# Optimization experiments

Measured on AMD Instinct MI355X. Metric: run time of the kernel, lower is better.

## Reference

```python
import jax, jax.numpy as jnp
import numpy as np

B, S, D, H, F = 16, 1024, 256, 8, 1024
HD = D // H  # head_dim = 32
EPS = 1e-5


def setup_inputs() -> dict:
    key = jax.random.key(0)
    ks = jax.random.split(key, 12)
    sc = 0.02
    return {
        "x":      jax.random.normal(ks[0], (B, S, D), dtype=jnp.float32),
        "gamma1": jnp.ones((S, D), dtype=jnp.float32),
        "beta1":  jnp.zeros((S, D), dtype=jnp.float32),
        "Wqkv":   jax.random.normal(ks[1], (3 * D, D), dtype=jnp.float32) * sc,
        "bqkv":   jnp.zeros((3 * D,), dtype=jnp.float32),
        "Wo":     jax.random.normal(ks[2], (D, D), dtype=jnp.float32) * sc,
        "bo":     jnp.zeros((D,), dtype=jnp.float32),
        "gamma2": jnp.ones((S, D), dtype=jnp.float32),
        "beta2":  jnp.zeros((S, D), dtype=jnp.float32),
        "W1":     jax.random.normal(ks[3], (F, D), dtype=jnp.float32) * sc,
        "b1":     jnp.zeros((F,), dtype=jnp.float32),
        "W2":     jax.random.normal(ks[4], (D, F), dtype=jnp.float32) * sc,
        "b2":     jnp.zeros((D,), dtype=jnp.float32),
    }


def _layernorm_2d(x, gamma, beta):
    # normalizes jointly over the last TWO dims (seq, d_model), biased variance
    mean = jnp.mean(x, axis=(-2, -1), keepdims=True)
    var = jnp.mean((x - mean) ** 2, axis=(-2, -1), keepdims=True)
    y = (x - mean) / jnp.sqrt(var + EPS)
    return gamma * y + beta


def _mha(x, Wqkv, bqkv, Wo, bo):
    b, s, d = x.shape
    qkv = x @ Wqkv.T + bqkv                                  # [B,S,3D]
    qkv = qkv.reshape(b, s, H, 3 * HD).transpose(0, 2, 1, 3)  # [B,H,S,3HD]
    q, k, v = jnp.split(qkv, 3, axis=-1)                      # each [B,H,S,HD]
    scores = jnp.einsum("bhqd,bhkd->bhqk", q, k) / np.sqrt(HD).astype(np.float32)
    attn = jax.nn.softmax(scores, axis=-1)                    # [B,H,S,S]
    values = jnp.einsum("bhqk,bhkd->bhqd", attn, v)           # [B,H,S,HD]
    # NOTE: original torch code reshapes (B,H,S,HD)->(B,S,H*HD) WITHOUT permuting
    # back; we faithfully reproduce that (row-major reshape, same as torch).
    values = values.reshape(b, s, H * HD)
    return values @ Wo.T + bo


def reference(x, gamma1, beta1, Wqkv, bqkv, Wo, bo, gamma2, beta2, W1, b1, W2, b2):
    # pre-norm attention block (dropout is identity at inference)
    h = _layernorm_2d(x, gamma1, beta1)
    h = _mha(h, Wqkv, bqkv, Wo, bo)
    x = x + h
    # pre-norm MLP block
    h = _layernorm_2d(x, gamma2, beta2)
    h = jax.nn.relu(h @ W1.T + b1) @ W2.T + b2
    return x + h
```

## Files before the change

kernel.cpp:

```cpp
#include <hip/hip_runtime.h>
#include <cstdint>
#include <cstddef>

#define SDn (1024*256)

typedef unsigned short u16;
typedef unsigned int   u32;
typedef __bf16 bf16x8 __attribute__((ext_vector_type(8)));
typedef u16    u16x4v __attribute__((ext_vector_type(4)));
typedef u32    u32x4v __attribute__((ext_vector_type(4)));
typedef float  f32x4  __attribute__((ext_vector_type(4)));
typedef float  f32x16 __attribute__((ext_vector_type(16)));

__device__ __forceinline__ u16 f2bf(float f){
  u32 u = __builtin_bit_cast(u32, f);
  u32 r = u + 0x7FFFu + ((u >> 16) & 1u);
  return (u16)(r >> 16);
}

#if __has_builtin(__builtin_amdgcn_exp2f)
#define EXP2(x) __builtin_amdgcn_exp2f(x)
#else
#define EXP2(x) exp2f(x)
#endif

__device__ __forceinline__ u32 cvtpk(float a, float b){
  u32 r;
  asm("v_cvt_pk_bf16_f32 %0, %1, %2" : "=v"(r) : "v"(a), "v"(b));
  return r;
}

__device__ __forceinline__ void gll16(const void* g, void* l){
  __builtin_amdgcn_global_load_lds((const __attribute__((address_space(1))) void*)g,
                                   (__attribute__((address_space(3))) void*)l, 16, 0, 0);
}

__global__ void prep(const float* __restrict__ x, float2* __restrict__ part,
                     const float* __restrict__ cw0, const float* __restrict__ cw1,
                     const float* __restrict__ cw2, const float* __restrict__ cw3,
                     u16* __restrict__ co0, u16* __restrict__ co1,
                     u16* __restrict__ co2, u16* __restrict__ co3)
{
  const int bid = blockIdx.x, t = threadIdx.x;
  if (bid < 768){
    int i = bid*256 + t;
    const float* src; u16* dst; int j = i;
    if      (j <  49152){ src = cw0; dst = co0; }
    else if (j <  65536){ src = cw1; dst = co1; j -=  49152; }
    else if (j < 131072){ src = cw2; dst = co2; j -=  65536; }
    else               { src = cw3; dst = co3; j -= 131072; }
    float4 v = ((const float4*)src)[j];
    u16x4v o; o[0]=f2bf(v.x); o[1]=f2bf(v.y); o[2]=f2bf(v.z); o[3]=f2bf(v.w);
    ((u16x4v*)dst)[j] = o;
    return;
  }
  __shared__ float2 red[4];
  const int i = bid - 768;
  const int b = i >> 6, c = i & 63;
  const float4* p = (const float4*)(x + (size_t)b*SDn + (size_t)c*4096);
  float s = 0.f, q = 0.f;
  #pragma unroll
  for (int k=0;k<4;k++){
    float4 v = p[t + k*256];
    s += v.x+v.y+v.z+v.w;
    q += v.x*v.x + v.y*v.y + v.z*v.z + v.w*v.w;
  }
  #pragma unroll
  for (int o=32;o;o>>=1){ s += __shfl_down(s,o); q += __shfl_down(q,o); }
  if ((t & 63) == 0) red[t>>6] = make_float2(s,q);
  __syncthreads();
  if (t == 0){
    float S=0.f,Q=0.f;
    #pragma unroll
    for (int k=0;k<4;k++){ S += red[k].x; Q += red[k].y; }
    part[b*64 + c] = make_float2(S,Q);
  }
}

__global__ void ln_apply(const float* __restrict__ x, const float* __restrict__ gamma,
                         const float* __restrict__ beta, const float2* __restrict__ part,
                         u16* __restrict__ y)
{
  int b = blockIdx.y, c = blockIdx.x, t = threadIdx.x;
  __shared__ float2 stat;
  if (t < 64){
    float2 v = part[b*64 + t];
    float s = v.x, q = v.y;
    #pragma unroll
    for (int o=32;o;o>>=1){ s += __shfl_down(s,o); q += __shfl_down(q,o); }
    if (t == 0){
      float mean = s / (float)SDn;
      float var  = q / (float)SDn - mean*mean;
      stat = make_float2(mean, rsqrtf(var + 1e-5f));
    }
  }
  __syncthreads();
  const float mean = stat.x, rstd = stat.y;
  const size_t off = (size_t)b*SDn + (size_t)c*4096;
  const float4* px = (const float4*)(x + off);
  const float4* pg = (const float4*)(gamma + (size_t)c*4096);
  const float4* pb = (const float4*)(beta  + (size_t)c*4096);
  u16x4v* py = (u16x4v*)(y + off);
  #pragma unroll
  for (int i=0;i<4;i++){
    float4 xv = px[t + i*256];
    float4 gv = pg[t + i*256];
    float4 bv = pb[t + i*256];
    u16x4v o;
    o[0] = f2bf(gv.x*(xv.x-mean)*rstd + bv.x);
    o[1] = f2bf(gv.y*(xv.y-mean)*rstd + bv.y);
    o[2] = f2bf(gv.z*(xv.z-mean)*rstd + bv.z);
    o[3] = f2bf(gv.w*(xv.w-mean)*rstd + bv.w);
    py[t + i*256] = o;
  }
}

__global__ void ln2_apply(const float* __restrict__ x, const float* __restrict__ gamma,
                          const float* __restrict__ beta, const float2* __restrict__ part2,
                          u16* __restrict__ y)
{
  int b = blockIdx.y, c = blockIdx.x, t = threadIdx.x;
  __shared__ float2 stat;
  if (t < 32){
    float2 v = part2[b*32 + t];
    float s = v.x, q = v.y;
    #pragma unroll
    for (int o=16;o;o>>=1){ s += __shfl_down(s,o); q += __shfl_down(q,o); }
    if (t == 0){
      float mean = s / (float)SDn;
      float var  = q / (float)SDn - mean*mean;
      stat = make_float2(mean, rsqrtf(var + 1e-5f));
    }
  }
  __syncthreads();
  const float mean = stat.x, rstd = stat.y;
  const size_t off = (size_t)b*SDn + (size_t)c*4096;
  const float4* px = (const float4*)(x + off);
  const float4* pg = (const float4*)(gamma + (size_t)c*4096);
  const float4* pb = (const float4*)(beta  + (size_t)c*4096);
  u16x4v* py = (u16x4v*)(y + off);
  #pragma unroll
  for (int i=0;i<4;i++){
    float4 xv = px[t + i*256];
    float4 gv = pg[t + i*256];
    float4 bv = pb[t + i*256];
    u16x4v o;
    o[0] = f2bf(gv.x*(xv.x-mean)*rstd + bv.x);
    o[1] = f2bf(gv.y*(xv.y-mean)*rstd + bv.y);
    o[2] = f2bf(gv.z*(xv.z-mean)*rstd + bv.z);
    o[3] = f2bf(gv.w*(xv.w-mean)*rstd + bv.w);
    py[t + i*256] = o;
  }
}

template<int EPI>
__launch_bounds__(256, 4)
__global__ void gemm128(const u16* __restrict__ A, const u16* __restrict__ W,
                        const float* __restrict__ bias,
                        u16* __restrict__ o0, u16* __restrict__ o1, u16* __restrict__ o2,
                        int K, int N)
{
  __shared__ u16 As[2][4096];
  __shared__ u16 Bs[2][4096];
  const int tid  = threadIdx.x;
  const int lane = tid & 63;
  const int wid  = tid >> 6;
  const int wm = wid >> 1, wn = wid & 1;
  const int g  = lane >> 4;
  const int lr = lane & 15;
  const int m0 = blockIdx.x * 128;
  const int n0 = blockIdx.y * 128;

  f32x4 zf = {0.f,0.f,0.f,0.f};
  f32x4 acc[4][4];
  #pragma unroll
  for (int i=0;i<4;i++)
    #pragma unroll
    for (int j=0;j<4;j++) acc[i][j] = zf;

  const int r0 = tid >> 2, c0 = tid & 3;
  const int cs = c0 ^ ((r0 >> 1) & 3);
  const u16* Ar0 = A + (size_t)(m0 + r0     )*K + cs*8;
  const u16* Ar1 = A + (size_t)(m0 + r0 + 64)*K + cs*8;
  const u16* Wr0 = W + (size_t)(n0 + r0     )*K + cs*8;
  const u16* Wr1 = W + (size_t)(n0 + r0 + 64)*K + cs*8;

  int aoff[4], boff[4];
  #pragma unroll
  for (int m=0;m<4;m++){
    int ra = wm*64 + m*16 + lr;
    aoff[m] = (ra*4 + (g ^ ((ra>>1)&3))) * 8;
    int rb = wn*64 + m*16 + lr;
    boff[m] = (rb*4 + (g ^ ((rb>>1)&3))) * 8;
  }

  auto STAGE = [&](int buf, int k0){
    gll16(Ar0 + k0, &As[buf][tid*8]);
    gll16(Ar1 + k0, &As[buf][(tid+256)*8]);
    gll16(Wr0 + k0, &Bs[buf][tid*8]);
    gll16(Wr1 + k0, &Bs[buf][(tid+256)*8]);
  };

  STAGE(0, 0);
  __syncthreads();
  int cur = 0;
  for (int k0 = 0; k0 < K; k0 += 32){
    if (k0 + 32 < K) STAGE(cur^1, k0 + 32);
    bf16x8 af[4], bfv[4];
    #pragma unroll
    for (int m=0;m<4;m++) af[m]  = *(const bf16x8*)(&As[cur][aoff[m]]);
    #pragma unroll
    for (int n=0;n<4;n++) bfv[n] = *(const bf16x8*)(&Bs[cur][boff[n]]);
    #pragma unroll
    for (int m=0;m<4;m++)
      #pragma unroll
      for (int n=0;n<4;n++)
        acc[m][n] = __builtin_amdgcn_mfma_f32_16x16x32_bf16(af[m], bfv[n], acc[m][n], 0, 0, 0);
    __syncthreads();
    cur ^= 1;
  }

  #pragma unroll
  for (int m=0;m<4;m++){
    const int rowb = m0 + wm*64 + m*16 + g*4;
    #pragma unroll
    for (int n=0;n<4;n++){
      const int col = n0 + wn*64 + n*16 + lr;
      const float bc = bias[col];
      if constexpr (EPI == 0){
        const int hh  = col / 96;
        const int rem = col - hh*96;
        const int which = rem >> 5;
        const int d = rem & 31;
        #pragma unroll
        for (int rr=0;rr<4;rr++){
          const int rw = rowb + rr;
          const int b = rw >> 10, s = rw & 1023;
          float v = acc[m][n][rr] + bc;
          if (which == 0)
            o0[((size_t)((b*8 + hh)*1024 + s))*32 + d] = f2bf(v * (0.17677669529663689f * 1.4426950408889634f));
          else if (which == 1)
            o1[((size_t)((b*8 + hh)*1024 + s))*32 + d] = f2bf(v);
          else
            o2[((size_t)((b*8 + hh)*32 + d))*1024 + s] = f2bf(v);
        }
      } else {
        #pragma unroll
        for (int rr=0;rr<4;rr++){
          float v = acc[m][n][rr] + bc;
          o0[(size_t)(rowb + rr) * N + col] = f2bf(v > 0.f ? v : 0.f);
        }
      }
    }
  }
}

template<int STATS>
__launch_bounds__(256, 4)
__global__ void gemm64(const u16* __restrict__ A, const u16* __restrict__ W,
                       const float* __restrict__ bias, const float* __restrict__ res,
                       float* __restrict__ outF, float2* __restrict__ part2,
                       int K, int N)
{
  __shared__ u16 As[2][2048];
  __shared__ u16 Bs[2][4096];
  __shared__ float2 sred[4];
  const int tid  = threadIdx.x;
  const int lane = tid & 63;
  const int wid  = tid >> 6;
  const int g  = lane >> 4;
  const int lr = lane & 15;
  const int m0 = blockIdx.x * 64;
  const int n0 = blockIdx.y * 128;

  f32x4 zf = {0.f,0.f,0.f,0.f};
  f32x4 acc[4][2];
  #pragma unroll
  for (int i=0;i<4;i++){ acc[i][0]=zf; acc[i][1]=zf; }

  const int r0 = tid >> 2, c0 = tid & 3;
  const int cs = c0 ^ ((r0 >> 1) & 3);
  const u16* Asrc  = A + (size_t)(m0 + r0)*K + cs*8;
  const u16* Wsrc0 = W + (size_t)(n0 + r0     )*K + cs*8;
  const u16* Wsrc1 = W + (size_t)(n0 + r0 + 64)*K + cs*8;

  int aoff[4], boff[2];
  #pragma unroll
  for (int m=0;m<4;m++){
    int ra = m*16 + lr;
    aoff[m] = (ra*4 + (g ^ ((ra>>1)&3))) * 8;
  }
  #pragma unroll
  for (int n=0;n<2;n++){
    int rb = wid*32 + n*16 + lr;
    boff[n] = (rb*4 + (g ^ ((rb>>1)&3))) * 8;
  }

  auto STAGE = [&](int buf, int k0){
    gll16(Asrc  + k0, &As[buf][tid*8]);
    gll16(Wsrc0 + k0, &Bs[buf][tid*8]);
    gll16(Wsrc1 + k0, &Bs[buf][(tid+256)*8]);
  };

  STAGE(0, 0);
  __syncthreads();
  int cur = 0;
  for (int k0 = 0; k0 < K; k0 += 32){
    if (k0 + 32 < K) STAGE(cur^1, k0 + 32);
    bf16x8 af[4], bfv[2];
    #pragma unroll
    for (int m=0;m<4;m++) af[m]  = *(const bf16x8*)(&As[cur][aoff[m]]);
    #pragma unroll
    for (int n=0;n<2;n++) bfv[n] = *(const bf16x8*)(&Bs[cur][boff[n]]);
    #pragma unroll
    for (int m=0;m<4;m++)
      #pragma unroll
      for (int n=0;n<2;n++)
        acc[m][n] = __builtin_amdgcn_mfma_f32_16x16x32_bf16(af[m], bfv[n], acc[m][n], 0, 0, 0);
    __syncthreads();
    cur ^= 1;
  }

  float s = 0.f, q = 0.f;
  #pragma unroll
  for (int m=0;m<4;m++){
    const int rowb = m0 + m*16 + g*4;
    #pragma unroll
    for (int n=0;n<2;n++){
      const int col = n0 + wid*32 + n*16 + lr;
      const float bc = bias[col];
      #pragma unroll
      for (int rr=0;rr<4;rr++){
        size_t idx = (size_t)(rowb + rr) * N + col;
        float v = res[idx] + acc[m][n][rr] + bc;
        outF[idx] = v;
        if constexpr (STATS){ s += v; q += v*v; }
      }
    }
  }

  if constexpr (STATS){
    #pragma unroll
    for (int o=32;o;o>>=1){ s += __shfl_down(s,o); q += __shfl_down(q,o); }
    if (lane == 0) sred[wid] = make_float2(s,q);
    __syncthreads();
    if (tid == 0){
      float S=0.f,Q=0.f;
      #pragma unroll
      for (int k=0;k<4;k++){ S += sred[k].x; Q += sred[k].y; }
      part2[blockIdx.x*2 + blockIdx.y] = make_float2(S,Q);
    }
  }
}

__launch_bounds__(256, 5)
__global__ void attn32(const u16* __restrict__ Q, const u16* __restrict__ Kb,
                       const u16* __restrict__ Vt, u16* __restrict__ vals)
{
  __shared__ u16 Ks[2][4096];
  __shared__ u16 Vs[2][4096];
  const int tid  = threadIdx.x;
  const int lane = tid & 63;
  const int wid  = tid >> 6;
  const int l31  = lane & 31;
  const int l5   = lane >> 5;
  const int bh = blockIdx.x;
  const int q0 = blockIdx.y * 128;
  const size_t base = (size_t)bh * (1024*32);

  const int qrow = q0 + wid*32 + l31;
  const bf16x8 qf0 = *(const bf16x8*)(Q + base + (size_t)qrow*32 + l5*8);
  const bf16x8 qf1 = *(const bf16x8*)(Q + base + (size_t)qrow*32 + 16 + l5*8);

  f32x16 acc = {};
  float lsum = 0.f;

  const int kr = tid >> 2, kc = tid & 3;
  const int vd = tid >> 4, vc = tid & 15;
  const u16* Ksrc0 = Kb + base + (size_t)(kr     )*32 + (kc ^ (kr&3))*8;
  const u16* Ksrc1 = Kb + base + (size_t)(kr + 64)*32 + (kc ^ (kr&3))*8;
  const u16* Vsrc0 = Vt + base + (size_t)(vd     )*1024 + (vc ^ (vd&15))*8;
  const u16* Vsrc1 = Vt + base + (size_t)(vd + 16)*1024 + (vc ^ (vd&15))*8;

  auto STAGE = [&](int buf, int kv0){
    gll16(Ksrc0 + (size_t)kv0*32, &Ks[buf][tid*8]);
    gll16(Ksrc1 + (size_t)kv0*32, &Ks[buf][(tid+256)*8]);
    gll16(Vsrc0 + kv0, &Vs[buf][tid*8]);
    gll16(Vsrc1 + kv0, &Vs[buf][(tid+256)*8]);
  };

  STAGE(0, 0);
  __syncthreads();
  int cur = 0;
  for (int kv0 = 0; kv0 < 1024; kv0 += 128){
    if (kv0 + 128 < 1024) STAGE(cur^1, kv0 + 128);

    #pragma unroll
    for (int G=0; G<4; ++G){
      const u16* ksb = &Ks[cur][(32*G + l31)*32];
      const int sw = l31 & 3;
      bf16x8 kf0 = *(const bf16x8*)(ksb + (((0|l5) ^ sw) << 3));
      bf16x8 kf1 = *(const bf16x8*)(ksb + (((2|l5) ^ sw) << 3));
      f32x16 sf = __builtin_amdgcn_mfma_f32_32x32x16_bf16(kf0, qf0, (f32x16){}, 0, 0, 0);
      sf = __builtin_amdgcn_mfma_f32_32x32x16_bf16(kf1, qf1, sf, 0, 0, 0);

      u32 W[8];
      #pragma unroll
      for (int j=0;j<4;j++){
        float p0 = EXP2(sf[4*j+0]);
        float p1 = EXP2(sf[4*j+1]);
        float p2 = EXP2(sf[4*j+2]);
        float p3 = EXP2(sf[4*j+3]);
        lsum += (p0 + p1) + (p2 + p3);
        W[2*j+0] = cvtpk(p0, p1);
        W[2*j+1] = cvtpk(p2, p3);
      }

      #pragma unroll
      for (int sl=0; sl<2; ++sl){
        u32 a0 = W[4*sl + 0], b0 = W[4*sl + 2];
        u32 a1 = W[4*sl + 1], b1 = W[4*sl + 3];
        asm("v_permlane32_swap_b32 %0, %1" : "+v"(a0), "+v"(b0));
        asm("v_permlane32_swap_b32 %0, %1" : "+v"(a1), "+v"(b1));
        bf16x8 pa = __builtin_bit_cast(bf16x8, (u32x4v){a0, a1, b0, b1});
        const int cp = 4*G + 2*sl + l5;
        bf16x8 vb = *(const bf16x8*)(&Vs[cur][l31*128 + ((cp ^ (l31 & 15)) << 3)]);
        acc = __builtin_amdgcn_mfma_f32_32x32x16_bf16(pa, vb, acc, 0, 0, 0);
      }
    }
    __syncthreads();
    cur ^= 1;
  }

  lsum += __shfl_xor(lsum, 32);
  float inv = 1.0f / lsum;

  const int b = bh >> 3, h = bh & 7;
  #pragma unroll
  for (int r=0;r<16;r++){
    int qloc = (r&3) + 8*(r>>2) + 4*l5;
    float iv = __shfl(inv, qloc);
    int sq = q0 + wid*32 + qloc;
    int srow = h*128 + (sq >> 3);
    vals[((size_t)b*1024 + srow)*256 + (sq&7)*32 + l31] = f2bf(acc[r] * iv);
  }
}

extern "C" void kernel_launch(void* const* d_in, const int* in_sizes, int n_in,
                              void* d_out, int out_size, void* d_ws, size_t ws_size,
                              hipStream_t stream)
{
  const float* x      = (const float*)d_in[0];
  const float* gamma1 = (const float*)d_in[1];
  const float* beta1  = (const float*)d_in[2];
  const float* Wqkv   = (const float*)d_in[3];
  const float* bqkv   = (const float*)d_in[4];
  const float* Wo     = (const float*)d_in[5];
  const float* bo     = (const float*)d_in[6];
  const float* gamma2 = (const float*)d_in[7];
  const float* beta2  = (const float*)d_in[8];
  const float* W1     = (const float*)d_in[9];
  const float* b1     = (const float*)d_in[10];
  const float* W2     = (const float*)d_in[11];
  const float* b2     = (const float*)d_in[12];
  float* out = (float*)d_out;
  char* ws = (char*)d_ws;

  float2* part  = (float2*)(ws + 256);
  float2* part2 = (float2*)(ws + 12288);
  u16* wq   = (u16*)(ws + 16384);
  u16* wo   = (u16*)(ws + 409600);
  u16* w1   = (u16*)(ws + 540672);
  u16* w2   = (u16*)(ws + 1064960);
  u16* hbuf = (u16*)(ws + 1589248);
  u16* qb   = (u16*)(ws + 9977856);
  u16* kb   = (u16*)(ws + 18366464);
  u16* vtb  = (u16*)(ws + 26755072);
  u16* valsb= (u16*)(ws + 35143680);
  u16* midb = (u16*)(ws + 9977856);

  prep<<<1792, 256, 0, stream>>>(x, part, Wqkv, Wo, W1, W2, wq, wo, w1, w2);

  ln_apply<<<dim3(64,16), 256, 0, stream>>>(x, gamma1, beta1, part, hbuf);

  gemm128<0><<<dim3(128,6), 256, 0, stream>>>(hbuf, wq, bqkv, qb, kb, vtb, 256, 768);

  attn32<<<dim3(128,8), 256, 0, stream>>>(qb, kb, vtb, valsb);

  gemm64<1><<<dim3(256,2), 256, 0, stream>>>(valsb, wo, bo, x, out, part2, 256, 256);

  ln2_apply<<<dim3(64,16), 256, 0, stream>>>(out, gamma2, beta2, part2, hbuf);

  gemm128<2><<<dim3(128,8), 256, 0, stream>>>(hbuf, w1, b1, midb, nullptr, nullptr, 256, 1024);

  gemm64<0><<<dim3(256,2), 256, 0, stream>>>(midb, w2, b2, out, out, nullptr, 1024, 256);
}
```

Before: 117.0 us.

## Store intermediate residual in bf16 and vectorize transposed V stores

The post-attention residual x1 is now written as bf16 to a new workspace buffer instead of fp32 to the output. ln2_apply and the final W2 GEMM read that bf16 copy, which cuts the memory traffic for the residual roughly in half across three kernels. The QKV GEMM epilogue also writes the transposed V tile as one 4-element vector store instead of four scalar stores. The cost is bf16 rounding on the residual path, which adds some error to the final output. The LayerNorm statistics are still accumulated in fp32 before rounding, so they no longer match the rounded values exactly.

```diff
diff --git a/kernel.cpp b/kernel.cpp
--- a/kernel.cpp
+++ b/kernel.cpp
@@ -16,6 +16,9 @@
   u32 u = __builtin_bit_cast(u32, f);
   u32 r = u + 0x7FFFu + ((u >> 16) & 1u);
   return (u16)(r >> 16);
+}
+__device__ __forceinline__ float bf2f(u16 v){
+  return __builtin_bit_cast(float, (u32)v << 16);
 }
 
 #if __has_builtin(__builtin_amdgcn_exp2f)
@@ -115,7 +118,7 @@
   }
 }
 
-__global__ void ln2_apply(const float* __restrict__ x, const float* __restrict__ gamma,
+__global__ void ln2_apply(const u16* __restrict__ x1b, const float* __restrict__ gamma,
                           const float* __restrict__ beta, const float2* __restrict__ part2,
                           u16* __restrict__ y)
 {
@@ -135,20 +138,20 @@
   __syncthreads();
   const float mean = stat.x, rstd = stat.y;
   const size_t off = (size_t)b*SDn + (size_t)c*4096;
-  const float4* px = (const float4*)(x + off);
+  const u16x4v* px = (const u16x4v*)(x1b + off);
   const float4* pg = (const float4*)(gamma + (size_t)c*4096);
   const float4* pb = (const float4*)(beta  + (size_t)c*4096);
   u16x4v* py = (u16x4v*)(y + off);
   #pragma unroll
   for (int i=0;i<4;i++){
-    float4 xv = px[t + i*256];
+    u16x4v xv = px[t + i*256];
     float4 gv = pg[t + i*256];
     float4 bv = pb[t + i*256];
     u16x4v o;
-    o[0] = f2bf(gv.x*(xv.x-mean)*rstd + bv.x);
-    o[1] = f2bf(gv.y*(xv.y-mean)*rstd + bv.y);
-    o[2] = f2bf(gv.z*(xv.z-mean)*rstd + bv.z);
-    o[3] = f2bf(gv.w*(xv.w-mean)*rstd + bv.w);
+    o[0] = f2bf(gv.x*(bf2f(xv[0])-mean)*rstd + bv.x);
+    o[1] = f2bf(gv.y*(bf2f(xv[1])-mean)*rstd + bv.y);
+    o[2] = f2bf(gv.z*(bf2f(xv[2])-mean)*rstd + bv.z);
+    o[3] = f2bf(gv.w*(bf2f(xv[3])-mean)*rstd + bv.w);
     py[t + i*256] = o;
   }
 }
@@ -232,17 +235,21 @@
         const int rem = col - hh*96;
         const int which = rem >> 5;
         const int d = rem & 31;
-        #pragma unroll
-        for (int rr=0;rr<4;rr++){
-          const int rw = rowb + rr;
-          const int b = rw >> 10, s = rw & 1023;
-          float v = acc[m][n][rr] + bc;
-          if (which == 0)
-            o0[((size_t)((b*8 + hh)*1024 + s))*32 + d] = f2bf(v * (0.17677669529663689f * 1.4426950408889634f));
-          else if (which == 1)
-            o1[((size_t)((b*8 + hh)*1024 + s))*32 + d] = f2bf(v);
-          else
-            o2[((size_t)((b*8 + hh)*32 + d))*1024 + s] = f2bf(v);
+        const int b = rowb >> 10, s0 = rowb & 1023;
+        if (which == 2){
+          u16x4v pv;
+          #pragma unroll
+          for (int rr=0;rr<4;rr++) pv[rr] = f2bf(acc[m][n][rr] + bc);
+          *(u16x4v*)(o2 + ((size_t)((b*8 + hh)*32 + d))*1024 + s0) = pv;
+        } else {
+          #pragma unroll
+          for (int rr=0;rr<4;rr++){
+            float v = acc[m][n][rr] + bc;
+            if (which == 0)
+              o0[((size_t)((b*8 + hh)*1024 + s0 + rr))*32 + d] = f2bf(v * (0.17677669529663689f * 1.4426950408889634f));
+            else
+              o1[((size_t)((b*8 + hh)*1024 + s0 + rr))*32 + d] = f2bf(v);
+          }
         }
       } else {
         #pragma unroll
@@ -255,11 +262,11 @@
   }
 }
 
-template<int STATS>
+template<int MODE>
 __launch_bounds__(256, 4)
 __global__ void gemm64(const u16* __restrict__ A, const u16* __restrict__ W,
-                       const float* __restrict__ bias, const float* __restrict__ res,
-                       float* __restrict__ outF, float2* __restrict__ part2,
+                       const float* __restrict__ bias, const void* __restrict__ resv,
+                       void* __restrict__ outv, float2* __restrict__ part2,
                        int K, int N)
 {
   __shared__ u16 As[2][2048];
@@ -332,14 +339,19 @@
       #pragma unroll
       for (int rr=0;rr<4;rr++){
         size_t idx = (size_t)(rowb + rr) * N + col;
-        float v = res[idx] + acc[m][n][rr] + bc;
-        outF[idx] = v;
-        if constexpr (STATS){ s += v; q += v*v; }
+        if constexpr (MODE == 1){
+          float v = ((const float*)resv)[idx] + acc[m][n][rr] + bc;
+          ((u16*)outv)[idx] = f2bf(v);
+          s += v; q += v*v;
+        } else {
+          float v = bf2f(((const u16*)resv)[idx]) + acc[m][n][rr] + bc;
+          ((float*)outv)[idx] = v;
+        }
       }
     }
   }
 
-  if constexpr (STATS){
+  if constexpr (MODE == 1){
     #pragma unroll
     for (int o=32;o;o>>=1){ s += __shfl_down(s,o); q += __shfl_down(q,o); }
     if (lane == 0) sred[wid] = make_float2(s,q);
@@ -478,6 +490,7 @@
   u16* vtb  = (u16*)(ws + 26755072);
   u16* valsb= (u16*)(ws + 35143680);
   u16* midb = (u16*)(ws + 9977856);
+  u16* x1b  = (u16*)(ws + 43532288);
 
   prep<<<1792, 256, 0, stream>>>(x, part, Wqkv, Wo, W1, W2, wq, wo, w1, w2);
 
@@ -487,11 +500,11 @@
 
   attn32<<<dim3(128,8), 256, 0, stream>>>(qb, kb, vtb, valsb);
 
-  gemm64<1><<<dim3(256,2), 256, 0, stream>>>(valsb, wo, bo, x, out, part2, 256, 256);
-
-  ln2_apply<<<dim3(64,16), 256, 0, stream>>>(out, gamma2, beta2, part2, hbuf);
+  gemm64<1><<<dim3(256,2), 256, 0, stream>>>(valsb, wo, bo, x, x1b, part2, 256, 256);
+
+  ln2_apply<<<dim3(64,16), 256, 0, stream>>>(x1b, gamma2, beta2, part2, hbuf);
 
   gemm128<2><<<dim3(128,8), 256, 0, stream>>>(hbuf, w1, b1, midb, nullptr, nullptr, 256, 1024);
 
-  gemm64<0><<<dim3(256,2), 256, 0, stream>>>(midb, w2, b2, out, out, nullptr, 1024, 256);
-}
+  gemm64<0><<<dim3(256,2), 256, 0, stream>>>(midb, w2, b2, x1b, out, nullptr, 1024, 256);
+}
```

Result: faster. 109.1 us (-6.8%).
